# Kernel tuning notes

Measured on AMD Instinct MI355X. Metric: run time of the kernel, lower is better.

Reference implementation:

```python
import jax, jax.numpy as jnp
import numpy as np

N_NODES = 100000
N_EDGES = 1600000
IN_DIM, HID, OUT_DIM = 5, 128, 1


def setup_inputs() -> dict:
    key = jax.random.key(0)
    ks = jax.random.split(key, 10)
    x = jax.random.normal(ks[0], (N_NODES, IN_DIM), dtype=jnp.float32)
    edge_index = jax.random.randint(ks[1], (2, N_EDGES), 0, N_NODES)
    s = lambda fi, fo: (2.0 / (fi + fo)) ** 0.5
    W1 = jax.random.normal(ks[2], (IN_DIM, HID), dtype=jnp.float32) * s(IN_DIM, HID)
    b1 = jnp.zeros((HID,), dtype=jnp.float32)
    W2 = jax.random.normal(ks[3], (HID, HID), dtype=jnp.float32) * s(HID, HID)
    b2 = jnp.zeros((HID,), dtype=jnp.float32)
    W3 = jax.random.normal(ks[4], (HID, HID), dtype=jnp.float32) * s(HID, HID)
    b3 = jnp.zeros((HID,), dtype=jnp.float32)
    Wfc = jax.random.normal(ks[5], (HID, OUT_DIM), dtype=jnp.float32) * s(HID, OUT_DIM)
    bfc = jnp.zeros((OUT_DIM,), dtype=jnp.float32)
    return {"x": x, "edge_index": edge_index, "W1": W1, "b1": b1,
            "W2": W2, "b2": b2, "W3": W3, "b3": b3, "Wfc": Wfc, "bfc": bfc}


def _gcn_norm(edge_index, n, dtype):
    # Add self-loops (PyG GCNConv default), then symmetric normalization.
    loops = jnp.arange(n)
    src = jnp.concatenate([edge_index[0], loops])
    dst = jnp.concatenate([edge_index[1], loops])
    deg = jax.ops.segment_sum(jnp.ones_like(dst, dtype=dtype), dst, num_segments=n)
    dinv = jnp.where(deg > 0, jax.lax.rsqrt(deg), 0.0)
    norm = dinv[src] * dinv[dst]  # [E+N]
    return src, dst, norm


def _gcn_conv(x, W, b, src, dst, norm, n):
    h = x @ W                      # linear transform first (PyG GCNConv)
    msg = h[src] * norm[:, None]   # gather + scale: [E+N, F]
    out = jax.ops.segment_sum(msg, dst, num_segments=n)  # scatter-add
    return out + b


def reference(x, edge_index, W1, b1, W2, b2, W3, b3, Wfc, bfc):
    n = x.shape[0]
    src, dst, norm = _gcn_norm(edge_index, n, x.dtype)
    h = jax.nn.relu(_gcn_conv(x, W1, b1, src, dst, norm, n))
    h = jax.nn.relu(_gcn_conv(h, W2, b2, src, dst, norm, n))
    h = jax.nn.relu(_gcn_conv(h, W3, b3, src, dst, norm, n))
    return h @ Wfc + bfc  # [N, OUT_DIM]
```

## Files before the change

kernel.cpp:

```cpp
#include <hip/hip_runtime.h>

#define N_NODES 100000
#define N_EDGES 1600000
#define HID 128
#define IN_DIM 5
#define XT_PITCH 132
#define BIN_SHIFT 9
#define BIN_NODES (1 << BIN_SHIFT)
#define NBINS ((N_NODES + BIN_NODES - 1) / BIN_NODES)
#define NBLK_P 256
#define EPB ((N_EDGES + NBLK_P - 1) / NBLK_P)
#define STAGE_CAP 12288


__global__ __launch_bounds__(256) void k_hist(const int* __restrict__ ei,
                                              int* __restrict__ cnt) {
    __shared__ int h[NBINS];
    int t = threadIdx.x, b = blockIdx.x;
    for (int i = t; i < NBINS; i += 256) h[i] = 0;
    __syncthreads();
    int e0 = b * EPB, e1 = e0 + EPB; if (e1 > N_EDGES) e1 = N_EDGES;
    for (int e = e0 + t; e < e1; e += 256)
        atomicAdd(&h[ei[N_EDGES + e] >> BIN_SHIFT], 1);
    __syncthreads();
    for (int i = t; i < NBINS; i += 256) cnt[b * NBINS + i] = h[i];
}

__global__ __launch_bounds__(256) void k_blkscan(const int* __restrict__ cnt,
                                                 int* __restrict__ ofs,
                                                 int* __restrict__ tot) {
    __shared__ int sm[NBLK_P];
    int bin = blockIdx.x, t = threadIdx.x;
    int v = cnt[t * NBINS + bin];
    sm[t] = v; __syncthreads();
    for (int off = 1; off < NBLK_P; off <<= 1) {
        int add = (t >= off) ? sm[t - off] : 0;
        __syncthreads();
        sm[t] += add;
        __syncthreads();
    }
    ofs[t * NBINS + bin] = sm[t] - v;
    if (t == NBLK_P - 1) tot[bin] = sm[t];
}

__global__ __launch_bounds__(256) void k_bin_scan(const int* __restrict__ tot,
                                                  int* __restrict__ bin_ofs) {
    __shared__ int sm[256];
    int t = threadIdx.x;
    int v = (t < NBINS) ? tot[t] : 0;
    sm[t] = v; __syncthreads();
    for (int off = 1; off < 256; off <<= 1) {
        int add = (t >= off) ? sm[t - off] : 0;
        __syncthreads();
        sm[t] += add;
        __syncthreads();
    }
    if (t < NBINS) bin_ofs[t] = sm[t] - v;
    if (t == 0) bin_ofs[NBINS] = N_EDGES;
}

__global__ __launch_bounds__(256) void k_scatter(const int* __restrict__ ei,
                                                 const int* __restrict__ ofs,
                                                 const int* __restrict__ bin_ofs,
                                                 int* __restrict__ bin_buf) {
    __shared__ int base[NBINS];
    __shared__ int lcnt[NBINS];
    int t = threadIdx.x, b = blockIdx.x;
    for (int i = t; i < NBINS; i += 256) {
        base[i] = bin_ofs[i] + ofs[b * NBINS + i];
        lcnt[i] = 0;
    }
    __syncthreads();
    int e0 = b * EPB, e1 = e0 + EPB; if (e1 > N_EDGES) e1 = N_EDGES;
    for (int e = e0 + t; e < e1; e += 256) {
        int s = ei[e], d = ei[N_EDGES + e];
        int bin = d >> BIN_SHIFT;
        int p = atomicAdd(&lcnt[bin], 1);
        bin_buf[base[bin] + p] = (s << BIN_SHIFT) | (d & (BIN_NODES - 1));
    }
}

__global__ __launch_bounds__(256) void k_fill2(const int* __restrict__ bin_buf,
                                               const int* __restrict__ bin_ofs,
                                               int* __restrict__ row_ptr,
                                               float* __restrict__ dinv,
                                               int* __restrict__ col) {
    __shared__ int cnt[BIN_NODES];
    __shared__ int excl[BIN_NODES];
    __shared__ int ps[256];
    __shared__ int stage[STAGE_CAP];
    int t = threadIdx.x, b = blockIdx.x;
    int node_base = b * BIN_NODES;
    int node_cnt = N_NODES - node_base; if (node_cnt > BIN_NODES) node_cnt = BIN_NODES;
    for (int i = t; i < BIN_NODES; i += 256) cnt[i] = 0;
    __syncthreads();
    int e0 = bin_ofs[b], e1 = bin_ofs[b + 1];
    for (int e = e0 + t; e < e1; e += 256)
        atomicAdd(&cnt[bin_buf[e] & (BIN_NODES - 1)], 1);
    __syncthreads();
    int a0 = cnt[2 * t], a1 = cnt[2 * t + 1];
    int psum = a0 + a1;
    ps[t] = psum; __syncthreads();
    for (int off = 1; off < 256; off <<= 1) {
        int add = (t >= off) ? ps[t - off] : 0;
        __syncthreads();
        ps[t] += add;
        __syncthreads();
    }
    int tbase = ps[t] - psum;
    excl[2 * t] = tbase;
    excl[2 * t + 1] = tbase + a0;
    __syncthreads();
    int row_base = bin_ofs[b];
    for (int i = t; i < node_cnt; i += 256) {
        row_ptr[node_base + i] = row_base + excl[i];
        dinv[node_base + i] = rsqrtf((float)(cnt[i] + 1));
    }
    if (b == NBINS - 1 && t == 0) row_ptr[N_NODES] = N_EDGES;
    __syncthreads();
    for (int i = t; i < BIN_NODES; i += 256) cnt[i] = excl[i];
    __syncthreads();
    for (int e = e0 + t; e < e1; e += 256) {
        int v = bin_buf[e];
        int p = atomicAdd(&cnt[v & (BIN_NODES - 1)], 1);
        int lsrc = v >> BIN_SHIFT;
        if (p < STAGE_CAP) stage[p] = lsrc;
        else col[row_base + p] = lsrc;
    }
    __syncthreads();
    int tote = e1 - e0; if (tote > STAGE_CAP) tote = STAGE_CAP;
    for (int i = t; i < tote; i += 256) col[row_base + i] = stage[i];
}


__global__ void k_xd(const float* __restrict__ x, const float* __restrict__ dinv,
                     float* __restrict__ xd) {
    int i = blockIdx.x * 256 + threadIdx.x;
    if (i < N_NODES * IN_DIM) xd[i] = x[i] * dinv[i / IN_DIM];
}


__global__ __launch_bounds__(256) void k_agg_x(const float* __restrict__ xd,
                                               const int* __restrict__ row_ptr,
                                               const int* __restrict__ col,
                                               float* __restrict__ sx) {
    int gw   = (blockIdx.x * 256 + threadIdx.x) >> 6;
    int lane = threadIdx.x & 63;
    int grp  = lane >> 3;
    int f    = lane & 7;
    int node = gw * 8 + grp;
    if (node >= N_NODES) return;
    bool act = (f < IN_DIM);
    float acc = act ? xd[node * IN_DIM + f] : 0.f;
    int j = row_ptr[node], end = row_ptr[node + 1];
    for (; j + 4 <= end; j += 4) {
        int s0 = col[j], s1 = col[j + 1], s2 = col[j + 2], s3 = col[j + 3];
        if (act) {
            float v0 = xd[s0 * IN_DIM + f];
            float v1 = xd[s1 * IN_DIM + f];
            float v2 = xd[s2 * IN_DIM + f];
            float v3 = xd[s3 * IN_DIM + f];
            acc += (v0 + v1) + (v2 + v3);
        }
    }
    for (; j < end; ++j) {
        int s = col[j];
        if (act) acc += xd[s * IN_DIM + f];
    }
    if (act) sx[node * IN_DIM + f] = acc;
}


__global__ void k_mm1f(const float* __restrict__ sx, const float* __restrict__ W1,
                       const float* __restrict__ b1, const float* __restrict__ dinv,
                       float* __restrict__ h) {
    __shared__ float Wl[IN_DIM * HID];
    __shared__ float bl[HID];
    int t = threadIdx.x;
    for (int j = t; j < IN_DIM * HID; j += 256) Wl[j] = W1[j];
    for (int j = t; j < HID; j += 256) bl[j] = b1[j];
    __syncthreads();
    int row = blockIdx.x * 2 + (t >> 7);
    int cc  = t & 127;
    float acc = 0.f;
    #pragma unroll
    for (int k = 0; k < IN_DIM; ++k)
        acc += sx[row * IN_DIM + k] * Wl[k * HID + cc];
    h[(size_t)row * HID + cc] = fmaxf(fmaf(dinv[row], acc, bl[cc]), 0.f);
}


__global__ __launch_bounds__(256) void k_mm_hid(const float* __restrict__ X,
                                                const float* __restrict__ W,
                                                const float* __restrict__ dinv,
                                                float* __restrict__ G) {
    __shared__ float Wl[64 * HID];
    __shared__ float xt[64 * XT_PITCH];
    int t = threadIdx.x;
    int row0 = blockIdx.x * 64;
    const float4* X4 = (const float4*)X;
    #pragma unroll
    for (int i = 0; i < 8; ++i) {
        int f = i * 256 + t;
        int r = f >> 5;
        int c = f & 31;
        float4 v = {0.f, 0.f, 0.f, 0.f};
        if (row0 + r < N_NODES) v = X4[(size_t)(row0 + r) * 32 + c];
        *(float4*)&xt[r * XT_PITCH + c * 4] = v;
    }
    const float4* Wg4 = (const float4*)W;
    float4* Wl4 = (float4*)Wl;
    int cg = t & 15;
    int rg = t >> 4;
    float4 acc[4][2] = {};
    for (int h = 0; h < 2; ++h) {
        __syncthreads();
        #pragma unroll
        for (int i = 0; i < 8; ++i) Wl4[i * 256 + t] = Wg4[h * 2048 + i * 256 + t];
        __syncthreads();
        #pragma unroll 4
        for (int kk = 0; kk < 64; kk += 4) {
            float4 xr[4];
            #pragma unroll
            for (int r = 0; r < 4; ++r)
                xr[r] = *(const float4*)&xt[(rg * 4 + r) * XT_PITCH + h * 64 + kk];
            #pragma unroll
            for (int q = 0; q < 4; ++q) {
                float4 w0 = Wl4[(kk + q) * 32 + cg * 2];
                float4 w1 = Wl4[(kk + q) * 32 + cg * 2 + 1];
                #pragma unroll
                for (int r = 0; r < 4; ++r) {
                    float xv = (q == 0) ? xr[r].x : (q == 1) ? xr[r].y
                             : (q == 2) ? xr[r].z : xr[r].w;
                    acc[r][0].x += xv * w0.x; acc[r][0].y += xv * w0.y;
                    acc[r][0].z += xv * w0.z; acc[r][0].w += xv * w0.w;
                    acc[r][1].x += xv * w1.x; acc[r][1].y += xv * w1.y;
                    acc[r][1].z += xv * w1.z; acc[r][1].w += xv * w1.w;
                }
            }
        }
    }
    #pragma unroll
    for (int r = 0; r < 4; ++r) {
        int row = row0 + rg * 4 + r;
        if (row < N_NODES) {
            float s = dinv[row];
            float4 a0 = acc[r][0], a1 = acc[r][1];
            a0.x *= s; a0.y *= s; a0.z *= s; a0.w *= s;
            a1.x *= s; a1.y *= s; a1.z *= s; a1.w *= s;
            float4* Gp = (float4*)(G + (size_t)row * HID + cg * 8);
            Gp[0] = a0; Gp[1] = a1;
        }
    }
}


template <int FINAL>
__global__ __launch_bounds__(256) void k_agg(const float* __restrict__ g,
                                             const int* __restrict__ row_ptr,
                                             const int* __restrict__ col,
                                             const float* __restrict__ dinv,
                                             const float* __restrict__ bias,
                                             const float* __restrict__ Wfc,
                                             const float* __restrict__ bfc,
                                             float* __restrict__ out) {
    int lane = threadIdx.x & 63;
    int w    = threadIdx.x >> 6;
    int node = blockIdx.x * 4 + w;
    const float2* g2 = (const float2*)g;
    float2 sacc = g2[(size_t)node * 64 + lane];
    float ax = sacc.x, ay = sacc.y;
    int start = row_ptr[node], end = row_ptr[node + 1];
    int idx = start + lane;
    int myc = (idx < end) ? col[idx] : 0;
    for (int j0 = start; j0 < end; j0 += 64) {
        int cur = myc;
        if (j0 + 64 < end) {
            int nidx = j0 + 64 + lane;
            myc = (nidx < end) ? col[nidx] : 0;
        }
        int cnt = end - j0; if (cnt > 64) cnt = 64;
        int jj = 0;
        for (; jj + 16 <= cnt; jj += 16) {
            int s[16];
            #pragma unroll
            for (int q = 0; q < 16; ++q) s[q] = __shfl(cur, jj + q);
            float2 v[16];
            #pragma unroll
            for (int q = 0; q < 16; ++q) v[q] = g2[(size_t)s[q] * 64 + lane];
            float px = 0.f, py = 0.f;
            #pragma unroll
            for (int q = 0; q < 16; ++q) { px += v[q].x; py += v[q].y; }
            ax += px; ay += py;
        }
        for (; jj + 4 <= cnt; jj += 4) {
            int s0 = __shfl(cur, jj);     int s1 = __shfl(cur, jj + 1);
            int s2 = __shfl(cur, jj + 2); int s3 = __shfl(cur, jj + 3);
            float2 v0 = g2[(size_t)s0 * 64 + lane];
            float2 v1 = g2[(size_t)s1 * 64 + lane];
            float2 v2 = g2[(size_t)s2 * 64 + lane];
            float2 v3 = g2[(size_t)s3 * 64 + lane];
            ax += (v0.x + v1.x) + (v2.x + v3.x);
            ay += (v0.y + v1.y) + (v2.y + v3.y);
        }
        for (; jj < cnt; ++jj) {
            int s = __shfl(cur, jj);
            float2 v = g2[(size_t)s * 64 + lane];
            ax += v.x; ay += v.y;
        }
    }
    float sc = dinv[node];
    float2 bb = *(const float2*)(bias + lane * 2);
    float o0 = fmaxf(fmaf(sc, ax, bb.x), 0.f);
    float o1 = fmaxf(fmaf(sc, ay, bb.y), 0.f);
    if (FINAL == 0) {
        *(float2*)(out + (size_t)node * HID + lane * 2) = make_float2(o0, o1);
    } else {
        float2 wv = *(const float2*)(Wfc + lane * 2);
        float d = o0 * wv.x + o1 * wv.y;
        #pragma unroll
        for (int off = 32; off > 0; off >>= 1) d += __shfl_down(d, off, 64);
        if (lane == 0) out[node] = d + bfc[0];
    }
}


extern "C" void kernel_launch(void* const* d_in, const int* in_sizes, int n_in,
                              void* d_out, int out_size, void* d_ws, size_t ws_size,
                              hipStream_t stream) {
    (void)in_sizes; (void)n_in; (void)out_size; (void)ws_size;
    const float* x   = (const float*)d_in[0];
    const int*   ei  = (const int*)d_in[1];
    const float* W1  = (const float*)d_in[2];
    const float* b1  = (const float*)d_in[3];
    const float* W2  = (const float*)d_in[4];
    const float* b2  = (const float*)d_in[5];
    const float* W3  = (const float*)d_in[6];
    const float* b3  = (const float*)d_in[7];
    const float* Wfc = (const float*)d_in[8];
    const float* bfc = (const float*)d_in[9];
    float* out = (float*)d_out;

    char* p = (char*)d_ws;
    auto alloc = [&](size_t bytes) -> void* {
        void* r = (void*)p;
        p += (bytes + 511) & ~(size_t)511;
        return r;
    };
    float* dinv    = (float*)alloc((size_t)N_NODES * 4);
    int*   row_ptr = (int*)  alloc((size_t)(N_NODES + 1) * 4);
    int*   cnt     = (int*)  alloc((size_t)NBLK_P * NBINS * 4);
    int*   ofs     = (int*)  alloc((size_t)NBLK_P * NBINS * 4);
    int*   tot     = (int*)  alloc((size_t)NBINS * 4);
    int*   bin_ofs = (int*)  alloc((size_t)(NBINS + 1) * 4);
    int*   col     = (int*)  alloc((size_t)N_EDGES * 4);
    float* bufA    = (float*)alloc((size_t)N_NODES * HID * 4);
    float* bufB    = (float*)alloc((size_t)N_NODES * HID * 4);
    int*   bin_buf = (int*)bufA;
    float* xd      = (float*)bufA;
    float* sx      = (float*)bufA + 512000;

    k_hist   <<<NBLK_P, 256, 0, stream>>>(ei, cnt);
    k_blkscan<<<NBINS, 256, 0, stream>>>(cnt, ofs, tot);
    k_bin_scan<<<1, 256, 0, stream>>>(tot, bin_ofs);
    k_scatter<<<NBLK_P, 256, 0, stream>>>(ei, ofs, bin_ofs, bin_buf);
    k_fill2  <<<NBINS, 256, 0, stream>>>(bin_buf, bin_ofs, row_ptr, dinv, col);

    int mm_blocks = (N_NODES + 63) / 64;

    k_xd   <<<(N_NODES * IN_DIM + 255) / 256, 256, 0, stream>>>(x, dinv, xd);
    k_agg_x<<<(N_NODES + 31) / 32, 256, 0, stream>>>(xd, row_ptr, col, sx);
    k_mm1f <<<N_NODES / 2, 256, 0, stream>>>(sx, W1, b1, dinv, bufB);

    k_mm_hid<<<mm_blocks, 256, 0, stream>>>(bufB, W2, dinv, bufA);
    k_agg<0><<<N_NODES / 4, 256, 0, stream>>>(bufA, row_ptr, col, dinv, b2,
                                              nullptr, nullptr, bufB);
    k_mm_hid<<<mm_blocks, 256, 0, stream>>>(bufB, W3, dinv, bufA);
    k_agg<1><<<N_NODES / 4, 256, 0, stream>>>(bufA, row_ptr, col, dinv, b3,
                                              Wfc, bfc, out);
}
```

Baseline: 471.9 us.

## Split hidden aggregation into four feature-quarter passes for cache locality

The aggregation kernels now run four times, each gathering a 32-float (128-byte) slice of every neighbor row, so the working set per pass (100k x 32 floats) is more likely to stay resident in L2/LLC during the random gathers. Each wave splits into two half-waves that take alternating edges and combine with a cross-lane shuffle. The final layer writes per-quarter partial dot products that a new reduction kernel sums with the bias. The hidden matmul also switches to smaller transposed, padded weight tiles loaded in four phases with an occupancy hint of 3 blocks per SM. The cost is four times as many launches, repeated reads of the CSR index arrays, and narrower per-lane loads.

```diff
diff --git a/kernel.cpp b/kernel.cpp
--- a/kernel.cpp
+++ b/kernel.cpp
@@ -138,7 +138,6 @@
     int i = blockIdx.x * 256 + threadIdx.x;
     if (i < N_NODES * IN_DIM) xd[i] = x[i] * dinv[i / IN_DIM];
 }
-
 
 __global__ __launch_bounds__(256) void k_agg_x(const float* __restrict__ xd,
                                                const int* __restrict__ row_ptr,
@@ -170,7 +169,6 @@
     if (act) sx[node * IN_DIM + f] = acc;
 }
 
-
 __global__ void k_mm1f(const float* __restrict__ sx, const float* __restrict__ W1,
                        const float* __restrict__ b1, const float* __restrict__ dinv,
                        float* __restrict__ h) {
@@ -190,44 +188,45 @@
 }
 
 
-__global__ __launch_bounds__(256) void k_mm_hid(const float* __restrict__ X,
-                                                const float* __restrict__ W,
-                                                const float* __restrict__ dinv,
-                                                float* __restrict__ G) {
-    __shared__ float Wl[64 * HID];
+__global__ __launch_bounds__(256, 3) void k_mm_hid(const float* __restrict__ X,
+                                                   const float* __restrict__ W,
+                                                   const float* __restrict__ dinv,
+                                                   float* __restrict__ G) {
     __shared__ float xt[64 * XT_PITCH];
+    __shared__ float4 WlT[32 * 33];
     int t = threadIdx.x;
     int row0 = blockIdx.x * 64;
     const float4* X4 = (const float4*)X;
     #pragma unroll
     for (int i = 0; i < 8; ++i) {
-        int f = i * 256 + t;
-        int r = f >> 5;
-        int c = f & 31;
+        int fidx = i * 256 + t;
+        int r = fidx >> 5, c = fidx & 31;
         float4 v = {0.f, 0.f, 0.f, 0.f};
         if (row0 + r < N_NODES) v = X4[(size_t)(row0 + r) * 32 + c];
         *(float4*)&xt[r * XT_PITCH + c * 4] = v;
     }
     const float4* Wg4 = (const float4*)W;
-    float4* Wl4 = (float4*)Wl;
-    int cg = t & 15;
-    int rg = t >> 4;
+    int cg = t & 15, rg = t >> 4;
     float4 acc[4][2] = {};
-    for (int h = 0; h < 2; ++h) {
+    for (int ph = 0; ph < 4; ++ph) {
         __syncthreads();
         #pragma unroll
-        for (int i = 0; i < 8; ++i) Wl4[i * 256 + t] = Wg4[h * 2048 + i * 256 + t];
-        __syncthreads();
-        #pragma unroll 4
-        for (int kk = 0; kk < 64; kk += 4) {
+        for (int i = 0; i < 4; ++i) {
+            int fidx = i * 256 + t;
+            int kk = fidx >> 5, c4 = fidx & 31;
+            WlT[c4 * 33 + kk] = Wg4[(ph * 32 + kk) * 32 + c4];
+        }
+        __syncthreads();
+        #pragma unroll 2
+        for (int kk4 = 0; kk4 < 32; kk4 += 4) {
             float4 xr[4];
             #pragma unroll
             for (int r = 0; r < 4; ++r)
-                xr[r] = *(const float4*)&xt[(rg * 4 + r) * XT_PITCH + h * 64 + kk];
+                xr[r] = *(const float4*)&xt[(rg * 4 + r) * XT_PITCH + ph * 32 + kk4];
             #pragma unroll
             for (int q = 0; q < 4; ++q) {
-                float4 w0 = Wl4[(kk + q) * 32 + cg * 2];
-                float4 w1 = Wl4[(kk + q) * 32 + cg * 2 + 1];
+                float4 w0 = WlT[cg * 33 + kk4 + q];
+                float4 w1 = WlT[(cg + 16) * 33 + kk4 + q];
                 #pragma unroll
                 for (int r = 0; r < 4; ++r) {
                     float xv = (q == 0) ? xr[r].x : (q == 1) ? xr[r].y
@@ -248,28 +247,28 @@
             float4 a0 = acc[r][0], a1 = acc[r][1];
             a0.x *= s; a0.y *= s; a0.z *= s; a0.w *= s;
             a1.x *= s; a1.y *= s; a1.z *= s; a1.w *= s;
-            float4* Gp = (float4*)(G + (size_t)row * HID + cg * 8);
-            Gp[0] = a0; Gp[1] = a1;
+            *(float4*)(G + (size_t)row * HID + cg * 4)      = a0;
+            *(float4*)(G + (size_t)row * HID + 64 + cg * 4) = a1;
         }
     }
 }
 
 
 template <int FINAL>
-__global__ __launch_bounds__(256) void k_agg(const float* __restrict__ g,
-                                             const int* __restrict__ row_ptr,
-                                             const int* __restrict__ col,
-                                             const float* __restrict__ dinv,
-                                             const float* __restrict__ bias,
-                                             const float* __restrict__ Wfc,
-                                             const float* __restrict__ bfc,
-                                             float* __restrict__ out) {
+__global__ __launch_bounds__(256) void k_agg_q(const float* __restrict__ g,
+                                               const int* __restrict__ row_ptr,
+                                               const int* __restrict__ col,
+                                               const float* __restrict__ dinv,
+                                               const float* __restrict__ bias,
+                                               const float* __restrict__ Wfc,
+                                               float* __restrict__ outp, int Q) {
     int lane = threadIdx.x & 63;
     int w    = threadIdx.x >> 6;
     int node = blockIdx.x * 4 + w;
-    const float2* g2 = (const float2*)g;
-    float2 sacc = g2[(size_t)node * 64 + lane];
-    float ax = sacc.x, ay = sacc.y;
+    int h = lane >> 5, f = lane & 31;
+    int qoff = Q * 32;
+    const float* gq = g + qoff;
+    float acc = (h == 0) ? gq[(size_t)node * HID + f] : 0.f;
     int start = row_ptr[node], end = row_ptr[node + 1];
     int idx = start + lane;
     int myc = (idx < end) ? col[idx] : 0;
@@ -282,46 +281,41 @@
         int cnt = end - j0; if (cnt > 64) cnt = 64;
         int jj = 0;
         for (; jj + 16 <= cnt; jj += 16) {
-            int s[16];
+            int s[8];
             #pragma unroll
-            for (int q = 0; q < 16; ++q) s[q] = __shfl(cur, jj + q);
-            float2 v[16];
+            for (int q = 0; q < 8; ++q) s[q] = __shfl(cur, jj + 2 * q + h);
+            float v[8];
             #pragma unroll
-            for (int q = 0; q < 16; ++q) v[q] = g2[(size_t)s[q] * 64 + lane];
-            float px = 0.f, py = 0.f;
-            #pragma unroll
-            for (int q = 0; q < 16; ++q) { px += v[q].x; py += v[q].y; }
-            ax += px; ay += py;
-        }
-        for (; jj + 4 <= cnt; jj += 4) {
-            int s0 = __shfl(cur, jj);     int s1 = __shfl(cur, jj + 1);
-            int s2 = __shfl(cur, jj + 2); int s3 = __shfl(cur, jj + 3);
-            float2 v0 = g2[(size_t)s0 * 64 + lane];
-            float2 v1 = g2[(size_t)s1 * 64 + lane];
-            float2 v2 = g2[(size_t)s2 * 64 + lane];
-            float2 v3 = g2[(size_t)s3 * 64 + lane];
-            ax += (v0.x + v1.x) + (v2.x + v3.x);
-            ay += (v0.y + v1.y) + (v2.y + v3.y);
-        }
-        for (; jj < cnt; ++jj) {
+            for (int q = 0; q < 8; ++q) v[q] = gq[(size_t)s[q] * HID + f];
+            acc += ((v[0] + v[1]) + (v[2] + v[3])) + ((v[4] + v[5]) + (v[6] + v[7]));
+        }
+        for (; jj + 2 <= cnt; jj += 2) {
+            int s = __shfl(cur, jj + h);
+            acc += gq[(size_t)s * HID + f];
+        }
+        if (jj < cnt) {
             int s = __shfl(cur, jj);
-            float2 v = g2[(size_t)s * 64 + lane];
-            ax += v.x; ay += v.y;
-        }
-    }
-    float sc = dinv[node];
-    float2 bb = *(const float2*)(bias + lane * 2);
-    float o0 = fmaxf(fmaf(sc, ax, bb.x), 0.f);
-    float o1 = fmaxf(fmaf(sc, ay, bb.y), 0.f);
+            if (h == 0) acc += gq[(size_t)s * HID + f];
+        }
+    }
+    acc += __shfl_xor(acc, 32, 64);
+    float val = fmaxf(fmaf(dinv[node], acc, bias[qoff + f]), 0.f);
     if (FINAL == 0) {
-        *(float2*)(out + (size_t)node * HID + lane * 2) = make_float2(o0, o1);
+        if (h == 0) outp[(size_t)node * HID + qoff + f] = val;
     } else {
-        float2 wv = *(const float2*)(Wfc + lane * 2);
-        float d = o0 * wv.x + o1 * wv.y;
+        float d = val * Wfc[qoff + f];
         #pragma unroll
-        for (int off = 32; off > 0; off >>= 1) d += __shfl_down(d, off, 64);
-        if (lane == 0) out[node] = d + bfc[0];
-    }
+        for (int off = 16; off > 0; off >>= 1) d += __shfl_down(d, off, 32);
+        if (lane == 0) outp[(size_t)Q * N_NODES + node] = d;
+    }
+}
+
+__global__ void k_fcred(const float* __restrict__ partials,
+                        const float* __restrict__ bfc, float* __restrict__ out) {
+    int i = blockIdx.x * 256 + threadIdx.x;
+    if (i < N_NODES)
+        out[i] = ((partials[i] + partials[N_NODES + i]) +
+                  (partials[2 * N_NODES + i] + partials[3 * N_NODES + i])) + bfc[0];
 }
 
 
@@ -347,15 +341,16 @@
         p += (bytes + 511) & ~(size_t)511;
         return r;
     };
-    float* dinv    = (float*)alloc((size_t)N_NODES * 4);
-    int*   row_ptr = (int*)  alloc((size_t)(N_NODES + 1) * 4);
-    int*   cnt     = (int*)  alloc((size_t)NBLK_P * NBINS * 4);
-    int*   ofs     = (int*)  alloc((size_t)NBLK_P * NBINS * 4);
-    int*   tot     = (int*)  alloc((size_t)NBINS * 4);
-    int*   bin_ofs = (int*)  alloc((size_t)(NBINS + 1) * 4);
-    int*   col     = (int*)  alloc((size_t)N_EDGES * 4);
-    float* bufA    = (float*)alloc((size_t)N_NODES * HID * 4);
-    float* bufB    = (float*)alloc((size_t)N_NODES * HID * 4);
+    float* dinv     = (float*)alloc((size_t)N_NODES * 4);
+    int*   row_ptr  = (int*)  alloc((size_t)(N_NODES + 1) * 4);
+    int*   cnt      = (int*)  alloc((size_t)NBLK_P * NBINS * 4);
+    int*   ofs      = (int*)  alloc((size_t)NBLK_P * NBINS * 4);
+    int*   tot      = (int*)  alloc((size_t)NBINS * 4);
+    int*   bin_ofs  = (int*)  alloc((size_t)(NBINS + 1) * 4);
+    int*   col      = (int*)  alloc((size_t)N_EDGES * 4);
+    float* partials = (float*)alloc((size_t)4 * N_NODES * 4);
+    float* bufA     = (float*)alloc((size_t)N_NODES * HID * 4);
+    float* bufB     = (float*)alloc((size_t)N_NODES * HID * 4);
     int*   bin_buf = (int*)bufA;
     float* xd      = (float*)bufA;
     float* sx      = (float*)bufA + 512000;
@@ -373,9 +368,12 @@
     k_mm1f <<<N_NODES / 2, 256, 0, stream>>>(sx, W1, b1, dinv, bufB);
 
     k_mm_hid<<<mm_blocks, 256, 0, stream>>>(bufB, W2, dinv, bufA);
-    k_agg<0><<<N_NODES / 4, 256, 0, stream>>>(bufA, row_ptr, col, dinv, b2,
-                                              nullptr, nullptr, bufB);
+    for (int q = 0; q < 4; ++q)
+        k_agg_q<0><<<N_NODES / 4, 256, 0, stream>>>(bufA, row_ptr, col, dinv, b2,
+                                                    nullptr, bufB, q);
     k_mm_hid<<<mm_blocks, 256, 0, stream>>>(bufB, W3, dinv, bufA);
-    k_agg<1><<<N_NODES / 4, 256, 0, stream>>>(bufA, row_ptr, col, dinv, b3,
-                                              Wfc, bfc, out);
-}
+    for (int q = 0; q < 4; ++q)
+        k_agg_q<1><<<N_NODES / 4, 256, 0, stream>>>(bufA, row_ptr, col, dinv, b3,
+                                                    Wfc, partials, q);
+    k_fcred<<<(N_NODES + 255) / 256, 256, 0, stream>>>(partials, bfc, out);
+}
```

Measured after the change: 602.2 us. 27.6% more time.

## Shrink hidden GEMM tile, stream transposed W in k-slices, narrow agg unroll

Applied to the files above, without the earlier changes.

The hidden-layer matmul now works on 48-row tiles with 3 rows per thread. It streams W in 16-row k-slices into a small transposed, padded LDS buffer instead of staging 64 full rows, which cuts LDS and register use so more blocks fit per CU (launch bounds now request 4). Output columns are split into two strided halves. The aggregation kernel's 16-wide gather unroll becomes 8-wide to lower register pressure. The trade-off is eight more barrier phases per block and less memory-level parallelism per wave in the gathers.

```diff
diff --git a/kernel.cpp b/kernel.cpp
--- a/kernel.cpp
+++ b/kernel.cpp
@@ -138,7 +138,6 @@
     int i = blockIdx.x * 256 + threadIdx.x;
     if (i < N_NODES * IN_DIM) xd[i] = x[i] * dinv[i / IN_DIM];
 }
-
 
 __global__ __launch_bounds__(256) void k_agg_x(const float* __restrict__ xd,
                                                const int* __restrict__ row_ptr,
@@ -170,7 +169,6 @@
     if (act) sx[node * IN_DIM + f] = acc;
 }
 
-
 __global__ void k_mm1f(const float* __restrict__ sx, const float* __restrict__ W1,
                        const float* __restrict__ b1, const float* __restrict__ dinv,
                        float* __restrict__ h) {
@@ -190,46 +188,47 @@
 }
 
 
-__global__ __launch_bounds__(256) void k_mm_hid(const float* __restrict__ X,
-                                                const float* __restrict__ W,
-                                                const float* __restrict__ dinv,
-                                                float* __restrict__ G) {
-    __shared__ float Wl[64 * HID];
-    __shared__ float xt[64 * XT_PITCH];
+__global__ __launch_bounds__(256, 4) void k_mm_hid(const float* __restrict__ X,
+                                                   const float* __restrict__ W,
+                                                   const float* __restrict__ dinv,
+                                                   float* __restrict__ G) {
+    __shared__ float xt[48 * XT_PITCH];
+    __shared__ float4 WlT[32 * 17];
     int t = threadIdx.x;
-    int row0 = blockIdx.x * 64;
+    int row0 = blockIdx.x * 48;
     const float4* X4 = (const float4*)X;
     #pragma unroll
-    for (int i = 0; i < 8; ++i) {
-        int f = i * 256 + t;
-        int r = f >> 5;
-        int c = f & 31;
+    for (int i = 0; i < 6; ++i) {
+        int fidx = i * 256 + t;
+        int r = fidx >> 5, c = fidx & 31;
         float4 v = {0.f, 0.f, 0.f, 0.f};
         if (row0 + r < N_NODES) v = X4[(size_t)(row0 + r) * 32 + c];
         *(float4*)&xt[r * XT_PITCH + c * 4] = v;
     }
     const float4* Wg4 = (const float4*)W;
-    float4* Wl4 = (float4*)Wl;
-    int cg = t & 15;
-    int rg = t >> 4;
-    float4 acc[4][2] = {};
-    for (int h = 0; h < 2; ++h) {
+    int cg = t & 15, rg = t >> 4;
+    float4 acc[3][2] = {};
+    for (int ph = 0; ph < 8; ++ph) {
         __syncthreads();
         #pragma unroll
-        for (int i = 0; i < 8; ++i) Wl4[i * 256 + t] = Wg4[h * 2048 + i * 256 + t];
-        __syncthreads();
-        #pragma unroll 4
-        for (int kk = 0; kk < 64; kk += 4) {
-            float4 xr[4];
+        for (int i = 0; i < 2; ++i) {
+            int fidx = i * 256 + t;
+            int kk = fidx >> 5, c4 = fidx & 31;
+            WlT[c4 * 17 + kk] = Wg4[(ph * 16 + kk) * 32 + c4];
+        }
+        __syncthreads();
+        #pragma unroll
+        for (int kk4 = 0; kk4 < 16; kk4 += 4) {
+            float4 xr[3];
             #pragma unroll
-            for (int r = 0; r < 4; ++r)
-                xr[r] = *(const float4*)&xt[(rg * 4 + r) * XT_PITCH + h * 64 + kk];
+            for (int r = 0; r < 3; ++r)
+                xr[r] = *(const float4*)&xt[(rg * 3 + r) * XT_PITCH + ph * 16 + kk4];
             #pragma unroll
             for (int q = 0; q < 4; ++q) {
-                float4 w0 = Wl4[(kk + q) * 32 + cg * 2];
-                float4 w1 = Wl4[(kk + q) * 32 + cg * 2 + 1];
+                float4 w0 = WlT[cg * 17 + kk4 + q];
+                float4 w1 = WlT[(cg + 16) * 17 + kk4 + q];
                 #pragma unroll
-                for (int r = 0; r < 4; ++r) {
+                for (int r = 0; r < 3; ++r) {
                     float xv = (q == 0) ? xr[r].x : (q == 1) ? xr[r].y
                              : (q == 2) ? xr[r].z : xr[r].w;
                     acc[r][0].x += xv * w0.x; acc[r][0].y += xv * w0.y;
@@ -241,15 +240,15 @@
         }
     }
     #pragma unroll
-    for (int r = 0; r < 4; ++r) {
-        int row = row0 + rg * 4 + r;
+    for (int r = 0; r < 3; ++r) {
+        int row = row0 + rg * 3 + r;
         if (row < N_NODES) {
             float s = dinv[row];
             float4 a0 = acc[r][0], a1 = acc[r][1];
             a0.x *= s; a0.y *= s; a0.z *= s; a0.w *= s;
             a1.x *= s; a1.y *= s; a1.z *= s; a1.w *= s;
-            float4* Gp = (float4*)(G + (size_t)row * HID + cg * 8);
-            Gp[0] = a0; Gp[1] = a1;
+            *(float4*)(G + (size_t)row * HID + cg * 4)      = a0;
+            *(float4*)(G + (size_t)row * HID + 64 + cg * 4) = a1;
         }
     }
 }
@@ -281,17 +280,21 @@
         }
         int cnt = end - j0; if (cnt > 64) cnt = 64;
         int jj = 0;
-        for (; jj + 16 <= cnt; jj += 16) {
-            int s[16];
-            #pragma unroll
-            for (int q = 0; q < 16; ++q) s[q] = __shfl(cur, jj + q);
-            float2 v[16];
-            #pragma unroll
-            for (int q = 0; q < 16; ++q) v[q] = g2[(size_t)s[q] * 64 + lane];
-            float px = 0.f, py = 0.f;
-            #pragma unroll
-            for (int q = 0; q < 16; ++q) { px += v[q].x; py += v[q].y; }
-            ax += px; ay += py;
+        for (; jj + 8 <= cnt; jj += 8) {
+            int s0 = __shfl(cur, jj);     int s1 = __shfl(cur, jj + 1);
+            int s2 = __shfl(cur, jj + 2); int s3 = __shfl(cur, jj + 3);
+            int s4 = __shfl(cur, jj + 4); int s5 = __shfl(cur, jj + 5);
+            int s6 = __shfl(cur, jj + 6); int s7 = __shfl(cur, jj + 7);
+            float2 v0 = g2[(size_t)s0 * 64 + lane];
+            float2 v1 = g2[(size_t)s1 * 64 + lane];
+            float2 v2 = g2[(size_t)s2 * 64 + lane];
+            float2 v3 = g2[(size_t)s3 * 64 + lane];
+            float2 v4 = g2[(size_t)s4 * 64 + lane];
+            float2 v5 = g2[(size_t)s5 * 64 + lane];
+            float2 v6 = g2[(size_t)s6 * 64 + lane];
+            float2 v7 = g2[(size_t)s7 * 64 + lane];
+            ax += ((v0.x + v1.x) + (v2.x + v3.x)) + ((v4.x + v5.x) + (v6.x + v7.x));
+            ay += ((v0.y + v1.y) + (v2.y + v3.y)) + ((v4.y + v5.y) + (v6.y + v7.y));
         }
         for (; jj + 4 <= cnt; jj += 4) {
             int s0 = __shfl(cur, jj);     int s1 = __shfl(cur, jj + 1);
@@ -347,15 +350,15 @@
         p += (bytes + 511) & ~(size_t)511;
         return r;
     };
-    float* dinv    = (float*)alloc((size_t)N_NODES * 4);
-    int*   row_ptr = (int*)  alloc((size_t)(N_NODES + 1) * 4);
-    int*   cnt     = (int*)  alloc((size_t)NBLK_P * NBINS * 4);
-    int*   ofs     = (int*)  alloc((size_t)NBLK_P * NBINS * 4);
-    int*   tot     = (int*)  alloc((size_t)NBINS * 4);
-    int*   bin_ofs = (int*)  alloc((size_t)(NBINS + 1) * 4);
-    int*   col     = (int*)  alloc((size_t)N_EDGES * 4);
-    float* bufA    = (float*)alloc((size_t)N_NODES * HID * 4);
-    float* bufB    = (float*)alloc((size_t)N_NODES * HID * 4);
+    float* dinv     = (float*)alloc((size_t)N_NODES * 4);
+    int*   row_ptr  = (int*)  alloc((size_t)(N_NODES + 1) * 4);
+    int*   cnt      = (int*)  alloc((size_t)NBLK_P * NBINS * 4);
+    int*   ofs      = (int*)  alloc((size_t)NBLK_P * NBINS * 4);
+    int*   tot      = (int*)  alloc((size_t)NBINS * 4);
+    int*   bin_ofs  = (int*)  alloc((size_t)(NBINS + 1) * 4);
+    int*   col      = (int*)  alloc((size_t)N_EDGES * 4);
+    float* bufA     = (float*)alloc((size_t)N_NODES * HID * 4);
+    float* bufB     = (float*)alloc((size_t)N_NODES * HID * 4);
     int*   bin_buf = (int*)bufA;
     float* xd      = (float*)bufA;
     float* sx      = (float*)bufA + 512000;
@@ -366,7 +369,7 @@
     k_scatter<<<NBLK_P, 256, 0, stream>>>(ei, ofs, bin_ofs, bin_buf);
     k_fill2  <<<NBINS, 256, 0, stream>>>(bin_buf, bin_ofs, row_ptr, dinv, col);
 
-    int mm_blocks = (N_NODES + 63) / 64;
+    int mm_blocks = (N_NODES + 47) / 48;
 
     k_xd   <<<(N_NODES * IN_DIM + 255) / 256, 256, 0, stream>>>(x, dinv, xd);
     k_agg_x<<<(N_NODES + 31) / 32, 256, 0, stream>>>(xd, row_ptr, col, sx);
```

Measured after the change: 442.5 us. 6.2% less time.
